# Kernel optimization log

Hardware: AMD Instinct MI355X
Metric: run time of the kernel (lower is better)

Reference implementation:

```python
import jax, jax.numpy as jnp
import numpy as np

HEADS = 9
QK = 64   # qk_embed_dim = in_dim // num_heads = 576 // 9
VD = 64   # v_dim
KVS = 2   # kv_stride


def conv3x3(x, w):
    return jax.lax.conv_general_dilated(
        x, w, (1, 1), 'SAME', dimension_numbers=('NCHW', 'OIHW', 'NCHW'))


def deform_conv3x3(x, offset, w):
    """Deformable conv v1, 3x3, stride 1, pad 1, 1 deformable group.
    x: (n,C,H,W); offset: (n,18,H,W) channel layout [dy0,dx0,dy1,dx1,...]; w: (O,C,3,3).
    """
    n, C, H, W = x.shape
    ky, kx = jnp.meshgrid(jnp.arange(3, dtype=x.dtype), jnp.arange(3, dtype=x.dtype), indexing='ij')
    ky = ky.reshape(9)
    kx = kx.reshape(9)
    off = offset.reshape(n, 9, 2, H, W)
    ys = jnp.arange(H, dtype=x.dtype)
    xs = jnp.arange(W, dtype=x.dtype)
    # sampling positions: out_pos - pad + kernel_pos + learned offset -> (n,9,H,W)
    py = ys[None, None, :, None] - 1.0 + ky[None, :, None, None] + off[:, :, 0]
    px = xs[None, None, None, :] - 1.0 + kx[None, :, None, None] + off[:, :, 1]
    y0 = jnp.floor(py)
    x0 = jnp.floor(px)
    dy = py - y0
    dx = px - x0
    xf = x.reshape(n, C, H * W)

    def gather(yi, xi):
        valid = ((yi >= 0) & (yi < H) & (xi >= 0) & (xi < W)).astype(x.dtype)
        yc = jnp.clip(yi, 0, H - 1).astype(jnp.int32)
        xc = jnp.clip(xi, 0, W - 1).astype(jnp.int32)
        idx = (yc * W + xc).reshape(n, 1, 9 * H * W)
        v = jnp.take_along_axis(xf, idx, axis=2).reshape(n, C, 9, H, W)
        return v * valid[:, None]

    samp = (((1 - dy) * (1 - dx))[:, None] * gather(y0, x0)
            + ((1 - dy) * dx)[:, None] * gather(y0, x0 + 1)
            + (dy * (1 - dx))[:, None] * gather(y0 + 1, x0)
            + (dy * dx)[:, None] * gather(y0 + 1, x0 + 1))  # (n,C,9,H,W)
    return jnp.einsum('ock,nckhw->nohw', w.reshape(w.shape[0], C, 9), samp)


def setup_inputs() -> dict:
    key = jax.random.key(0)
    ks = jax.random.split(key, 10)
    n, C, H, W = 2, 576, 64, 64
    s1 = 1.0 / np.sqrt(C)
    s9 = 1.0 / np.sqrt(C * 9)
    return {
        'x': jax.random.normal(ks[0], (n, C, H, W), jnp.float32),
        'key_w': jax.random.normal(ks[1], (C, C), jnp.float32) * s1,
        'offset_w': jax.random.normal(ks[2], (18, C, 3, 3), jnp.float32) * 0.01,
        'dconv_w': jax.random.normal(ks[3], (C, C, 3, 3), jnp.float32) * s9,
        'value_w': jax.random.normal(ks[4], (C, C), jnp.float32) * s1,
        'proj_w': jax.random.normal(ks[5], (C, C), jnp.float32) * s1,
        'proj_b': jax.random.normal(ks[6], (C,), jnp.float32) * 0.01,
        'appr_bias': jax.random.normal(ks[7], (C,), jnp.float32) * s1,
        'appr_bias_q': jax.random.normal(ks[8], (C,), jnp.float32) * s1,
        'gamma': jax.random.normal(ks[9], (1,), jnp.float32) * 0.1,
    }


def reference(x, key_w, offset_w, dconv_w, value_w, proj_w, proj_b, appr_bias, appr_bias_q, gamma):
    n, C, H, W = x.shape
    x_q = x                              # q_stride == 1
    x_kv = x[:, :, ::KVS, ::KVS]         # AvgPool2d(kernel=1, stride=2)
    hk, wk = x_kv.shape[2], x_kv.shape[3]
    # key content term (appr_bias . key): per-kv scalar per head
    proj_key = jnp.einsum('oc,nchw->nohw', key_w, x_kv).reshape(n, HEADS, QK, hk * wk)
    b = jnp.einsum('he,nhek->nhk', appr_bias.reshape(HEADS, QK), proj_key)
    # query relative-position term via deformable conv: per-query scalar per head
    offset = conv3x3(x_q, offset_w)
    pq = deform_conv3x3(x_q, offset, dconv_w).reshape(n, HEADS, QK, H * W)
    a = jnp.einsum('he,nheq->nhq', appr_bias_q.reshape(HEADS, QK), pq)
    # energy (n, heads, HW, hk*wk); attention_type[0] is False so energy is a+b broadcast
    energy = a[..., :, None] + b[..., None, :]
    attn = jax.nn.softmax(energy, axis=-1)
    v = jnp.einsum('oc,nchw->nohw', value_w, x_kv).reshape(n, HEADS, VD, hk * wk)
    out = jnp.einsum('nhqk,nhdk->nhdq', attn, v).reshape(n, HEADS * VD, H, W)
    out = jnp.einsum('oc,nchw->nohw', proj_w, out) + proj_b[None, :, None, None]
    return gamma * out + x
```

## Files before the change

kernel.cpp:

```cpp
#include <hip/hip_runtime.h>


#define CCH 576
#define NHEADS 9
#define HW 4096
#define KHW 1024
#define WID 64
#define CH_CHUNKS 16
#define CH_PER 36

#define WS_BPART 0
#define WS_P     294912
#define WS_WX    313344
#define WS_OV    323712
#define WS_PO    324864

__global__ void k_bpart(const float* __restrict__ x, const float* __restrict__ key_w,
                        const float* __restrict__ appr_bias, float* __restrict__ bpart) {
    int k  = blockIdx.x * 256 + threadIdx.x;
    int n  = blockIdx.y;
    int ch = blockIdx.z;
    int c0 = ch * CH_PER;

    __shared__ float ab[CCH];
    __shared__ float kbs[NHEADS][CH_PER];
    for (int i = threadIdx.x; i < CCH; i += 256) ab[i] = appr_bias[i];
    __syncthreads();
    for (int t = threadIdx.x; t < NHEADS * CH_PER; t += 256) {
        int h = t / CH_PER, cl = t % CH_PER;
        float s = 0.f;
        #pragma unroll 8
        for (int e = 0; e < 64; ++e)
            s += ab[h * 64 + e] * key_w[(size_t)(h * 64 + e) * CCH + c0 + cl];
        kbs[h][cl] = s;
    }
    __syncthreads();

    int ky = k >> 5, kx = k & 31;
    const float* xb = x + (size_t)n * CCH * HW + (size_t)(ky * 2) * WID + kx * 2;
    float acc[NHEADS];
    #pragma unroll
    for (int h = 0; h < NHEADS; ++h) acc[h] = 0.f;
    for (int cl = 0; cl < CH_PER; ++cl) {
        float xv = xb[(size_t)(c0 + cl) * HW];
        #pragma unroll
        for (int h = 0; h < NHEADS; ++h) acc[h] += kbs[h][cl] * xv;
    }
    #pragma unroll
    for (int h = 0; h < NHEADS; ++h)
        bpart[(((size_t)n * CH_CHUNKS + ch) * NHEADS + h) * KHW + k] = acc[h];
}

__global__ void k_softmax(const float* __restrict__ bpart, float* __restrict__ p) {
    int nh = blockIdx.x;
    int n = nh / NHEADS, h = nh % NHEADS;
    int tid = threadIdx.x;
    int wave = tid >> 6, lane = tid & 63;
    float s[4];
    #pragma unroll
    for (int j = 0; j < 4; ++j) {
        int k = tid + j * 256;
        float v = 0.f;
        #pragma unroll
        for (int ch = 0; ch < CH_CHUNKS; ++ch)
            v += bpart[(((size_t)n * CH_CHUNKS + ch) * NHEADS + h) * KHW + k];
        s[j] = v;
    }
    float m = fmaxf(fmaxf(s[0], s[1]), fmaxf(s[2], s[3]));
    #pragma unroll
    for (int off = 32; off >= 1; off >>= 1)
        m = fmaxf(m, __shfl_xor(m, off, 64));
    __shared__ float redm[4];
    if (lane == 0) redm[wave] = m;
    __syncthreads();
    m = fmaxf(fmaxf(redm[0], redm[1]), fmaxf(redm[2], redm[3]));
    float e[4], lsum = 0.f;
    #pragma unroll
    for (int j = 0; j < 4; ++j) { e[j] = __expf(s[j] - m); lsum += e[j]; }
    #pragma unroll
    for (int off = 32; off >= 1; off >>= 1)
        lsum += __shfl_xor(lsum, off, 64);
    __shared__ float reds[4];
    if (lane == 0) reds[wave] = lsum;
    __syncthreads();
    float inv = 1.f / (reds[0] + reds[1] + reds[2] + reds[3]);
    #pragma unroll
    for (int j = 0; j < 4; ++j)
        p[(size_t)nh * KHW + tid + j * 256] = e[j] * inv;
}

__global__ void k_wx(const float* __restrict__ x, const float* __restrict__ p,
                     float* __restrict__ wx) {
    int n = blockIdx.y;
    __shared__ float ps[NHEADS * KHW];
    for (int i = threadIdx.x; i < NHEADS * KHW; i += 256)
        ps[i] = p[(size_t)n * NHEADS * KHW + i];
    __syncthreads();
    int wave = threadIdx.x >> 6, lane = threadIdx.x & 63;
    int c = blockIdx.x * 4 + wave;
    const float* xb = x + ((size_t)n * CCH + c) * HW;
    float acc[NHEADS];
    #pragma unroll
    for (int h = 0; h < NHEADS; ++h) acc[h] = 0.f;
    #pragma unroll 4
    for (int j = 0; j < 16; ++j) {
        int k = lane + 64 * j;
        int ky = k >> 5, kx = k & 31;
        float xv = xb[(size_t)(ky * 2) * WID + kx * 2];
        #pragma unroll
        for (int h = 0; h < NHEADS; ++h) acc[h] += ps[h * KHW + k] * xv;
    }
    #pragma unroll
    for (int h = 0; h < NHEADS; ++h) {
        float v = acc[h];
        #pragma unroll
        for (int off = 32; off >= 1; off >>= 1)
            v += __shfl_xor(v, off, 64);
        if (lane == 0) wx[((size_t)n * NHEADS + h) * CCH + c] = v;
    }
}

__global__ void k_ov(const float* __restrict__ value_w, const float* __restrict__ wx,
                     float* __restrict__ ov) {
    int g = blockIdx.x * 4 + (threadIdx.x >> 6);
    int lane = threadIdx.x & 63;
    int n = g / CCH, o = g % CCH;
    int h = o >> 6;
    float acc = 0.f;
    #pragma unroll
    for (int j = 0; j < 9; ++j) {
        int c = lane + 64 * j;
        acc += value_w[(size_t)o * CCH + c] * wx[((size_t)n * NHEADS + h) * CCH + c];
    }
    #pragma unroll
    for (int off = 32; off >= 1; off >>= 1)
        acc += __shfl_xor(acc, off, 64);
    if (lane == 0) ov[n * CCH + o] = acc;
}

__global__ void k_po(const float* __restrict__ proj_w, const float* __restrict__ proj_b,
                     const float* __restrict__ ov, float* __restrict__ po) {
    int g = blockIdx.x * 4 + (threadIdx.x >> 6);
    int lane = threadIdx.x & 63;
    int n = g / CCH, o = g % CCH;
    float acc = 0.f;
    #pragma unroll
    for (int j = 0; j < 9; ++j) {
        int c = lane + 64 * j;
        acc += proj_w[(size_t)o * CCH + c] * ov[n * CCH + c];
    }
    #pragma unroll
    for (int off = 32; off >= 1; off >>= 1)
        acc += __shfl_xor(acc, off, 64);
    if (lane == 0) po[n * CCH + o] = acc + proj_b[o];
}

__global__ void k_final(const float* __restrict__ x, const float* __restrict__ po,
                        const float* __restrict__ gamma, float* __restrict__ out) {
    const size_t total4 = (size_t)2 * CCH * HW / 4;
    float g = gamma[0];
    const float4* x4 = (const float4*)x;
    float4* o4 = (float4*)out;
    for (size_t i = (size_t)blockIdx.x * blockDim.x + threadIdx.x; i < total4;
         i += (size_t)gridDim.x * blockDim.x) {
        int no = (int)((i * 4) / HW);
        float base = g * po[no];
        float4 v = x4[i];
        v.x += base; v.y += base; v.z += base; v.w += base;
        o4[i] = v;
    }
}

extern "C" void kernel_launch(void* const* d_in, const int* in_sizes, int n_in,
                              void* d_out, int out_size, void* d_ws, size_t ws_size,
                              hipStream_t stream) {
    const float* x         = (const float*)d_in[0];
    const float* key_w     = (const float*)d_in[1];
    const float* value_w   = (const float*)d_in[4];
    const float* proj_w    = (const float*)d_in[5];
    const float* proj_b    = (const float*)d_in[6];
    const float* appr_bias = (const float*)d_in[7];
    const float* gamma     = (const float*)d_in[9];
    float* out = (float*)d_out;

    float* ws    = (float*)d_ws;
    float* bpart = ws + WS_BPART;
    float* p     = ws + WS_P;
    float* wx    = ws + WS_WX;
    float* ov    = ws + WS_OV;
    float* po    = ws + WS_PO;

    k_bpart  <<<dim3(4, 2, CH_CHUNKS), 256, 0, stream>>>(x, key_w, appr_bias, bpart);
    k_softmax<<<18, 256, 0, stream>>>(bpart, p);
    k_wx     <<<dim3(144, 2), 256, 0, stream>>>(x, p, wx);
    k_ov     <<<288, 256, 0, stream>>>(value_w, wx, ov);
    k_po     <<<288, 256, 0, stream>>>(proj_w, proj_b, ov, po);
    k_final  <<<2048, 256, 0, stream>>>(x, po, gamma, out);
}
```

Baseline: 37.51 us.

## Fuse softmax into weighted-sum kernel and projection into final residual kernel

Merges the softmax kernel into the weighted x-reduction kernel, so each of the 288 blocks recomputes the chunk-sum and softmax for all 9 heads in shared memory instead of reading a precomputed probability buffer. Also fuses the output projection dot product into the residual-add kernel, with one block per (n, channel) computing its bias scalar and then streaming that channel row. This removes two kernel launches and their intermediate global buffers, at the cost of redundant bpart reads and softmax work in every swx block.

```diff
diff --git a/kernel.cpp b/kernel.cpp
--- a/kernel.cpp
+++ b/kernel.cpp
@@ -2,32 +2,30 @@
 
 
 #define CCH 576
-#define NHEADS 9
+#define NH 9
 #define HW 4096
 #define KHW 1024
-#define WID 64
-#define CH_CHUNKS 16
-#define CH_PER 36
+#define W 64
+#define CHN 16
+#define CPC 36
 
 #define WS_BPART 0
-#define WS_P     294912
-#define WS_WX    313344
-#define WS_OV    323712
-#define WS_PO    324864
+#define WS_WX    294912
+#define WS_OV    (294912 + 10368)
 
 __global__ void k_bpart(const float* __restrict__ x, const float* __restrict__ key_w,
                         const float* __restrict__ appr_bias, float* __restrict__ bpart) {
     int k  = blockIdx.x * 256 + threadIdx.x;
     int n  = blockIdx.y;
     int ch = blockIdx.z;
-    int c0 = ch * CH_PER;
+    int c0 = ch * CPC;
 
     __shared__ float ab[CCH];
-    __shared__ float kbs[NHEADS][CH_PER];
+    __shared__ float kbs[NH][CPC];
     for (int i = threadIdx.x; i < CCH; i += 256) ab[i] = appr_bias[i];
     __syncthreads();
-    for (int t = threadIdx.x; t < NHEADS * CH_PER; t += 256) {
-        int h = t / CH_PER, cl = t % CH_PER;
+    for (int t = threadIdx.x; t < NH * CPC; t += 256) {
+        int h = t / CPC, cl = t % CPC;
         float s = 0.f;
         #pragma unroll 8
         for (int e = 0; e < 64; ++e)
@@ -37,86 +35,78 @@
     __syncthreads();
 
     int ky = k >> 5, kx = k & 31;
-    const float* xb = x + (size_t)n * CCH * HW + (size_t)(ky * 2) * WID + kx * 2;
-    float acc[NHEADS];
+    const float* xb = x + (size_t)n * CCH * HW + (size_t)(ky * 2) * W + kx * 2;
+    float acc[NH];
     #pragma unroll
-    for (int h = 0; h < NHEADS; ++h) acc[h] = 0.f;
-    for (int cl = 0; cl < CH_PER; ++cl) {
+    for (int h = 0; h < NH; ++h) acc[h] = 0.f;
+    for (int cl = 0; cl < CPC; ++cl) {
         float xv = xb[(size_t)(c0 + cl) * HW];
         #pragma unroll
-        for (int h = 0; h < NHEADS; ++h) acc[h] += kbs[h][cl] * xv;
+        for (int h = 0; h < NH; ++h) acc[h] += kbs[h][cl] * xv;
     }
     #pragma unroll
-    for (int h = 0; h < NHEADS; ++h)
-        bpart[(((size_t)n * CH_CHUNKS + ch) * NHEADS + h) * KHW + k] = acc[h];
+    for (int h = 0; h < NH; ++h)
+        bpart[(((size_t)n * CHN + ch) * NH + h) * KHW + k] = acc[h];
 }
 
-__global__ void k_softmax(const float* __restrict__ bpart, float* __restrict__ p) {
-    int nh = blockIdx.x;
-    int n = nh / NHEADS, h = nh % NHEADS;
+__global__ void k_swx(const float* __restrict__ x, const float* __restrict__ bpart,
+                      float* __restrict__ wx) {
+    int n = blockIdx.y;
     int tid = threadIdx.x;
-    int wave = tid >> 6, lane = tid & 63;
-    float s[4];
-    #pragma unroll
-    for (int j = 0; j < 4; ++j) {
-        int k = tid + j * 256;
+    int wv = tid >> 6, ln = tid & 63;
+    __shared__ float sm[NH * KHW];
+
+    const float* bp = bpart + (size_t)n * CHN * NH * KHW;
+    for (int i = tid; i < NH * KHW; i += 256) {
         float v = 0.f;
         #pragma unroll
-        for (int ch = 0; ch < CH_CHUNKS; ++ch)
-            v += bpart[(((size_t)n * CH_CHUNKS + ch) * NHEADS + h) * KHW + k];
-        s[j] = v;
+        for (int ch = 0; ch < CHN; ++ch)
+            v += bp[(size_t)ch * NH * KHW + i];
+        sm[i] = v;
     }
-    float m = fmaxf(fmaxf(s[0], s[1]), fmaxf(s[2], s[3]));
+    __syncthreads();
+
+    for (int h = wv; h < NH; h += 4) {
+        float* row = sm + h * KHW;
+        float m = -1e30f;
+        #pragma unroll
+        for (int j = 0; j < 16; ++j) m = fmaxf(m, row[ln + 64 * j]);
+        #pragma unroll
+        for (int off = 32; off >= 1; off >>= 1) m = fmaxf(m, __shfl_xor(m, off, 64));
+        float s = 0.f;
+        #pragma unroll
+        for (int j = 0; j < 16; ++j) {
+            float e = __expf(row[ln + 64 * j] - m);
+            row[ln + 64 * j] = e;
+            s += e;
+        }
+        #pragma unroll
+        for (int off = 32; off >= 1; off >>= 1) s += __shfl_xor(s, off, 64);
+        float inv = 1.f / s;
+        #pragma unroll
+        for (int j = 0; j < 16; ++j) row[ln + 64 * j] *= inv;
+    }
+    __syncthreads();
+
+    int c = blockIdx.x * 4 + wv;
+    const float* xb = x + ((size_t)n * CCH + c) * HW;
+    float acc[NH];
     #pragma unroll
-    for (int off = 32; off >= 1; off >>= 1)
-        m = fmaxf(m, __shfl_xor(m, off, 64));
-    __shared__ float redm[4];
-    if (lane == 0) redm[wave] = m;
-    __syncthreads();
-    m = fmaxf(fmaxf(redm[0], redm[1]), fmaxf(redm[2], redm[3]));
-    float e[4], lsum = 0.f;
-    #pragma unroll
-    for (int j = 0; j < 4; ++j) { e[j] = __expf(s[j] - m); lsum += e[j]; }
-    #pragma unroll
-    for (int off = 32; off >= 1; off >>= 1)
-        lsum += __shfl_xor(lsum, off, 64);
-    __shared__ float reds[4];
-    if (lane == 0) reds[wave] = lsum;
-    __syncthreads();
-    float inv = 1.f / (reds[0] + reds[1] + reds[2] + reds[3]);
-    #pragma unroll
-    for (int j = 0; j < 4; ++j)
-        p[(size_t)nh * KHW + tid + j * 256] = e[j] * inv;
-}
-
-__global__ void k_wx(const float* __restrict__ x, const float* __restrict__ p,
-                     float* __restrict__ wx) {
-    int n = blockIdx.y;
-    __shared__ float ps[NHEADS * KHW];
-    for (int i = threadIdx.x; i < NHEADS * KHW; i += 256)
-        ps[i] = p[(size_t)n * NHEADS * KHW + i];
-    __syncthreads();
-    int wave = threadIdx.x >> 6, lane = threadIdx.x & 63;
-    int c = blockIdx.x * 4 + wave;
-    const float* xb = x + ((size_t)n * CCH + c) * HW;
-    float acc[NHEADS];
-    #pragma unroll
-    for (int h = 0; h < NHEADS; ++h) acc[h] = 0.f;
+    for (int h = 0; h < NH; ++h) acc[h] = 0.f;
     #pragma unroll 4
     for (int j = 0; j < 16; ++j) {
-        int k = lane + 64 * j;
+        int k = ln + 64 * j;
         int ky = k >> 5, kx = k & 31;
-        float xv = xb[(size_t)(ky * 2) * WID + kx * 2];
+        float xv = xb[(size_t)(ky * 2) * W + kx * 2];
         #pragma unroll
-        for (int h = 0; h < NHEADS; ++h) acc[h] += ps[h * KHW + k] * xv;
+        for (int h = 0; h < NH; ++h) acc[h] += sm[h * KHW + k] * xv;
     }
     #pragma unroll
-    for (int h = 0; h < NHEADS; ++h) {
+    for (int h = 0; h < NH; ++h) {
         float v = acc[h];
         #pragma unroll
-        for (int off = 32; off >= 1; off >>= 1)
-            v += __shfl_xor(v, off, 64);
-        if (lane == 0) wx[((size_t)n * NHEADS + h) * CCH + c] = v;
+        for (int off = 32; off >= 1; off >>= 1) v += __shfl_xor(v, off, 64);
+        if (ln == 0) wx[((size_t)n * NH + h) * CCH + c] = v;
     }
 }
 
@@ -126,48 +116,46 @@
     int lane = threadIdx.x & 63;
     int n = g / CCH, o = g % CCH;
     int h = o >> 6;
+    const float* vw  = value_w + (size_t)o * CCH;
+    const float* wxr = wx + ((size_t)n * NH + h) * CCH;
     float acc = 0.f;
     #pragma unroll
-    for (int j = 0; j < 9; ++j) {
-        int c = lane + 64 * j;
-        acc += value_w[(size_t)o * CCH + c] * wx[((size_t)n * NHEADS + h) * CCH + c];
-    }
+    for (int j = 0; j < 9; ++j)
+        acc += vw[lane + 64 * j] * wxr[lane + 64 * j];
     #pragma unroll
     for (int off = 32; off >= 1; off >>= 1)
         acc += __shfl_xor(acc, off, 64);
     if (lane == 0) ov[n * CCH + o] = acc;
 }
 
-__global__ void k_po(const float* __restrict__ proj_w, const float* __restrict__ proj_b,
-                     const float* __restrict__ ov, float* __restrict__ po) {
-    int g = blockIdx.x * 4 + (threadIdx.x >> 6);
-    int lane = threadIdx.x & 63;
-    int n = g / CCH, o = g % CCH;
-    float acc = 0.f;
-    #pragma unroll
-    for (int j = 0; j < 9; ++j) {
-        int c = lane + 64 * j;
-        acc += proj_w[(size_t)o * CCH + c] * ov[n * CCH + c];
-    }
+__global__ void k_pofinal(const float* __restrict__ proj_w, const float* __restrict__ proj_b,
+                          const float* __restrict__ ov, const float* __restrict__ x,
+                          const float* __restrict__ gamma, float* __restrict__ out) {
+    int b = blockIdx.x;
+    int n = b / CCH, o = b % CCH;
+    int t = threadIdx.x;
+    int wv = t >> 6, ln = t & 63;
+    __shared__ float pr[4];
+
+    const float* pw  = proj_w + (size_t)o * CCH;
+    const float* ovr = ov + n * CCH;
+    float acc = pw[t] * ovr[t] + pw[t + 256] * ovr[t + 256];
+    if (t < 64) acc += pw[t + 512] * ovr[t + 512];
     #pragma unroll
     for (int off = 32; off >= 1; off >>= 1)
         acc += __shfl_xor(acc, off, 64);
-    if (lane == 0) po[n * CCH + o] = acc + proj_b[o];
-}
+    if (ln == 0) pr[wv] = acc;
+    __syncthreads();
+    float base = gamma[0] * ((pr[0] + pr[1] + pr[2] + pr[3]) + proj_b[o]);
 
-__global__ void k_final(const float* __restrict__ x, const float* __restrict__ po,
-                        const float* __restrict__ gamma, float* __restrict__ out) {
-    const size_t total4 = (size_t)2 * CCH * HW / 4;
-    float g = gamma[0];
-    const float4* x4 = (const float4*)x;
-    float4* o4 = (float4*)out;
-    for (size_t i = (size_t)blockIdx.x * blockDim.x + threadIdx.x; i < total4;
-         i += (size_t)gridDim.x * blockDim.x) {
-        int no = (int)((i * 4) / HW);
-        float base = g * po[no];
-        float4 v = x4[i];
+    const float4* x4 = (const float4*)(x + ((size_t)n * CCH + o) * HW);
+    float4* o4 = (float4*)(out + ((size_t)n * CCH + o) * HW);
+    #pragma unroll
+    for (int j = 0; j < 4; ++j) {
+        int idx = t + 256 * j;
+        float4 v = x4[idx];
         v.x += base; v.y += base; v.z += base; v.w += base;
-        o4[i] = v;
+        o4[idx] = v;
     }
 }
 
@@ -185,15 +173,11 @@
 
     float* ws    = (float*)d_ws;
     float* bpart = ws + WS_BPART;
-    float* p     = ws + WS_P;
     float* wx    = ws + WS_WX;
     float* ov    = ws + WS_OV;
-    float* po    = ws + WS_PO;
 
-    k_bpart  <<<dim3(4, 2, CH_CHUNKS), 256, 0, stream>>>(x, key_w, appr_bias, bpart);
-    k_softmax<<<18, 256, 0, stream>>>(bpart, p);
-    k_wx     <<<dim3(144, 2), 256, 0, stream>>>(x, p, wx);
+    k_bpart  <<<dim3(4, 2, CHN), 256, 0, stream>>>(x, key_w, appr_bias, bpart);
+    k_swx    <<<dim3(144, 2), 256, 0, stream>>>(x, bpart, wx);
     k_ov     <<<288, 256, 0, stream>>>(value_w, wx, ov);
-    k_po     <<<288, 256, 0, stream>>>(proj_w, proj_b, ov, po);
-    k_final  <<<2048, 256, 0, stream>>>(x, po, gamma, out);
+    k_pofinal<<<1152, 256, 0, stream>>>(proj_w, proj_b, ov, x, gamma, out);
 }
```

Result: slower. 52.31 us (+39.5%).
